# Optimization experiments

Hardware: AMD Instinct MI355X
Metric: run time of the kernel (lower is better)

## Reference

```python
import jax, jax.numpy as jnp
import numpy as np

N_QUBITS = 10
DEPTH = 2
CNOT_PATTERN = [(i, i + 1) for i in range(N_QUBITS - 1)] + [(N_QUBITS - 1, 0)]

def _signs(n):
    # Pauli-Z eigenvalue (+1/-1) of each basis state for each wire; wire 0 = MSB
    idx = np.arange(2 ** n)
    bits = (idx[:, None] >> np.arange(n - 1, -1, -1)[None, :]) & 1
    return jnp.asarray(1.0 - 2.0 * bits, jnp.float32)  # [2^n, n]

SIGNS = _signs(N_QUBITS)

def _apply_rx(s, theta, wire):
    # s: [B, 2,2,...,2] complex; RX(theta) = [[c, -i s],[-i s, c]], c=cos(theta/2)
    s0 = jnp.take(s, 0, axis=wire + 1)
    s1 = jnp.take(s, 1, axis=wire + 1)
    c = jnp.cos(theta * 0.5)
    sn = jnp.sin(theta * 0.5)
    if c.ndim:  # per-batch angle -> broadcast over remaining wire axes
        shp = (-1,) + (1,) * (s0.ndim - 1)
        c = c.reshape(shp)
        sn = sn.reshape(shp)
    return jnp.stack([c * s0 - 1j * sn * s1, -1j * sn * s0 + c * s1], axis=wire + 1)

def _apply_cnot(s, src, tgt):
    # flip target wire on the src=1 subspace (X gate == flip of the size-2 axis)
    s0 = jnp.take(s, 0, axis=src + 1)
    s1 = jnp.take(s, 1, axis=src + 1)
    t_ax = tgt + 1 - (1 if tgt > src else 0)  # target axis after removing src axis
    s1 = jnp.flip(s1, axis=t_ax)
    return jnp.stack([s0, s1], axis=src + 1)

def _qgate(x, rx_params):
    # x: [B, n_qubits] data angles -> PauliZ expectations [B, n_qubits]
    B = x.shape[0]
    n = N_QUBITS
    s = jnp.zeros((B, 2 ** n), jnp.complex64).at[:, 0].set(1.0)
    s = s.reshape((B,) + (2,) * n)
    for w in range(n):
        s = _apply_rx(s, x[:, w], w)
    for _ in range(DEPTH):
        for w in range(n):
            s = _apply_rx(s, rx_params[w], w)
        for src, tgt in CNOT_PATTERN:
            s = _apply_cnot(s, src, tgt)
    probs = jnp.abs(s.reshape(B, -1)) ** 2  # [B, 2^n]
    return probs @ SIGNS  # [B, n]


def setup_inputs():
    key = jax.random.key(0)
    ks = jax.random.split(key, 10)
    T, B, D, H = 256, 256, 128, N_QUBITS
    fan_in = D + H
    sc = 1.0 / np.sqrt(fan_in)
    def lin(k1, k2):
        W = jax.random.uniform(k1, (H, fan_in), jnp.float32, -sc, sc)
        b = jax.random.uniform(k2, (H,), jnp.float32, -sc, sc)
        return W, b
    inputs = jax.random.normal(ks[0], (T, B, D), jnp.float32)
    rx_params = jax.random.normal(ks[1], (H,), jnp.float32)
    Wf, bf = lin(ks[2], ks[3])
    Wi, bi = lin(ks[4], ks[5])
    Wg, bg = lin(ks[6], ks[7])
    Wo, bo = lin(ks[8], ks[9])
    return dict(inputs=inputs, rx_params=rx_params, Wf=Wf, bf=bf, Wi=Wi, bi=bi,
                Wg=Wg, bg=bg, Wo=Wo, bo=bo)


def reference(inputs, rx_params, Wf, bf, Wi, bi, Wg, bg, Wo, bo):
    T, B, _ = inputs.shape
    H = N_QUBITS
    def step(carry, x_t):
        hx, cx = carry
        comb = jnp.concatenate([x_t, hx], axis=1)  # [B, D+H]
        f = jax.nn.sigmoid(_qgate(comb @ Wf.T + bf, rx_params))
        i = jax.nn.sigmoid(_qgate(comb @ Wi.T + bi, rx_params))
        g = jnp.tanh(_qgate(comb @ Wg.T + bg, rx_params))
        o = jax.nn.sigmoid(_qgate(comb @ Wo.T + bo, rx_params))
        cx = f * cx + i * g
        hx = o * jnp.tanh(cx)
        return (hx, cx), hx
    h0 = jnp.zeros((B, H), inputs.dtype)
    c0 = jnp.zeros((B, H), inputs.dtype)
    (hT, cT), ys = jax.lax.scan(step, (h0, c0), inputs)
    return ys, hT, cT
```

## Files before the change

kernel.cpp:

```cpp
#include <hip/hip_runtime.h>
#include <math.h>

#define T_STEPS 256
#define BATCH   256
#define DDIM    128
#define NH      10

typedef float v2f __attribute__((ext_vector_type(2)));
__device__ __forceinline__ v2f sp(float x){ v2f r; r.x = x; r.y = x; return r; }
#define PKFMA(a,b,c) __builtin_elementwise_fma((a),(b),(c))

template<int CTRL, int RMASK, int BMASK>
__device__ __forceinline__ float dppz(float x){
  return __int_as_float(__builtin_amdgcn_update_dpp(
      0, __float_as_int(x), CTRL, RMASK, BMASK, true));
}
__device__ __forceinline__ float red63(float v){
  v += dppz<0x111, 0xF, 0xF>(v);
  v += dppz<0x112, 0xF, 0xF>(v);
  v += dppz<0x114, 0xF, 0xE>(v);
  v += dppz<0x118, 0xF, 0xC>(v);
  v += dppz<0x142, 0xA, 0xF>(v);
  v += dppz<0x143, 0xC, 0xF>(v);
  return v;
}
__device__ __forceinline__ float rdlane(float v, int l){
  return __int_as_float(__builtin_amdgcn_readlane(__float_as_int(v), l));
}

template<int CTRL,int RMASK,int BMASK>
__device__ __forceinline__ float lad_add(float v){ return v + dppz<CTRL,RMASK,BMASK>(v); }
template<int CTRL,int RMASK,int BMASK>
__device__ __forceinline__ float lad_sub(float v){ return dppz<CTRL,RMASK,BMASK>(v) - v; }
#define LAD0_A(v) lad_add<0x111,0xF,0xF>(v)
#define LAD0_S(v) lad_sub<0x111,0xF,0xF>(v)
#define LAD1_A(v) lad_add<0x112,0xF,0xF>(v)
#define LAD1_S(v) lad_sub<0x112,0xF,0xF>(v)
#define LAD2_A(v) lad_add<0x114,0xF,0xE>(v)
#define LAD2_S(v) lad_sub<0x114,0xF,0xE>(v)
#define LAD3_A(v) lad_add<0x118,0xF,0xC>(v)
#define LAD3_S(v) lad_sub<0x118,0xF,0xC>(v)
#define LAD4_A(v) lad_add<0x142,0xA,0xF>(v)
#define LAD4_S(v) lad_sub<0x142,0xA,0xF>(v)
#define LAD5_A(v) lad_add<0x143,0xC,0xF>(v)
#define LAD5_S(v) lad_sub<0x143,0xC,0xF>(v)

__device__ __forceinline__ float dsx32(float x){ return __shfl_xor(x, 32, 64); }
__device__ __forceinline__ float dsx16(float x){
  return __int_as_float(__builtin_amdgcn_ds_swizzle(__float_as_int(x), 0x401F));
}
__device__ __forceinline__ float dsx8(float x){
  return __int_as_float(__builtin_amdgcn_ds_swizzle(__float_as_int(x), 0x201F));
}
__device__ __forceinline__ float dsx4(float x){
  return __int_as_float(__builtin_amdgcn_ds_swizzle(__float_as_int(x), 0x101F));
}
__device__ __forceinline__ float dsx2(float x){
  return __int_as_float(__builtin_amdgcn_ds_swizzle(__float_as_int(x), 0x081F));
}
__device__ __forceinline__ float dsx1(float x){
  return __int_as_float(__builtin_amdgcn_ds_swizzle(__float_as_int(x), 0x041F));
}

#define NK 4

#define RX_LANE_T(FETCH, tv)                                                   \
  { const v2f tt_ = sp(tv), nt_ = sp(-(tv));                                   \
    _Pragma("unroll")                                                          \
    for (int k = 0; k < NK; ++k){                                              \
      v2f oa, ob;                                                              \
      oa.x = FETCH(RE[k].x); oa.y = FETCH(RE[k].y);                            \
      ob.x = FETCH(IM[k].x); ob.y = FETCH(IM[k].y);                            \
      RE[k] = PKFMA(tt_, ob, RE[k]);                                           \
      IM[k] = PKFMA(nt_, oa, IM[k]);                                           \
    } }

template<int XB>
__device__ __forceinline__ void rx_reg_t(float tv, v2f* RE, v2f* IM){
  const v2f tt = sp(tv), nt = sp(-tv);
  v2f oR[NK], oI[NK];
  #pragma unroll
  for (int k = 0; k < NK; ++k){ oR[k] = RE[k]; oI[k] = IM[k]; }
  #pragma unroll
  for (int k = 0; k < NK; ++k){
    RE[k] = PKFMA(tt, oI[k ^ XB], RE[k]);
    IM[k] = PKFMA(nt, oR[k ^ XB], IM[k]);
  }
}
__device__ __forceinline__ void rx_reg9_t(float tv, v2f* RE, v2f* IM){
  const v2f tt = sp(tv), nt = sp(-tv);
  #pragma unroll
  for (int k = 0; k < NK; ++k){
    v2f oa = __builtin_shufflevector(RE[k], RE[k], 1, 0);
    v2f ob = __builtin_shufflevector(IM[k], IM[k], 1, 0);
    RE[k] = PKFMA(tt, ob, RE[k]);
    IM[k] = PKFMA(nt, oa, IM[k]);
  }
}

__device__ __forceinline__ void xdots(float xa, float xb,
                                      const v2f* WA, const v2f* WB, float* s){
  v2f xav = sp(xa), xbv = sp(xb);
  v2f p0 = PKFMA(xav, WA[0], xbv * WB[0]);
  v2f p1 = PKFMA(xav, WA[1], xbv * WB[1]);
  v2f p2 = PKFMA(xav, WA[2], xbv * WB[2]);
  s[0] = red63(p0.x); s[1] = red63(p0.y);
  s[2] = red63(p1.x); s[3] = red63(p1.y);
  s[4] = red63(p2.x);
}

__global__ void __launch_bounds__(512)
__attribute__((amdgpu_waves_per_eu(2)))
qlstm_kernel(const float* __restrict__ inp, const float* __restrict__ rxp,
             const float* __restrict__ Wf, const float* __restrict__ bf,
             const float* __restrict__ Wi, const float* __restrict__ bi,
             const float* __restrict__ Wg, const float* __restrict__ bg,
             const float* __restrict__ Wo, const float* __restrict__ bo,
             float* __restrict__ out)
{
  const int b    = blockIdx.x;
  const int tid  = threadIdx.x;
  const int wv   = tid >> 6;
  const int g    = wv >> 1;
  const int half = wv & 1;
  const int lane = tid & 63;

  __shared__ float4 Sx[4][2][4][64];
  __shared__ float4 partv[2][64];
  __shared__ float xpub_s[4][16];
  ((float*)partv)[tid] = 0.f;

  const float* Wp = (g == 0) ? Wf : (g == 1) ? Wi : (g == 2) ? Wg : Wo;
  const float* bp = (g == 0) ? bf : (g == 1) ? bi : (g == 2) ? bg : bo;

  const float WSC = 0.07957747154594767f;

  const int wbase = half * 5;
  v2f WA[3], WB[3];
  float bq[5];
  #pragma unroll
  for (int k = 0; k < 5; ++k) bq[k] = WSC * (bp[wbase + k] + rxp[wbase + k]);
  #pragma unroll
  for (int j = 0; j < 3; ++j){
    const int w0 = wbase + 2*j, w1 = wbase + 2*j + 1;
    WA[j].x = WSC * Wp[w0*138 + lane];
    WB[j].x = WSC * Wp[w0*138 + 64 + lane];
    if (2*j + 1 < 5){
      WA[j].y = WSC * Wp[w1*138 + lane];
      WB[j].y = WSC * Wp[w1*138 + 64 + lane];
    } else { WA[j].y = 0.f; WB[j].y = 0.f; }
  }
  float wCT[NH];
  {
    const int row = (lane < NH) ? lane : 0;
    #pragma unroll
    for (int j = 0; j < NH; ++j){
      float v = WSC * Wp[row*138 + 128 + j];
      wCT[j] = (lane < NH) ? v : 0.f;
    }
  }

  float tq[NH];
  float PC = 1.f;
  #pragma unroll
  for (int w = 0; w < NH; ++w){
    float th = 0.5f * rxp[w];
    float cw = cosf(th), sw = sinf(th);
    PC *= cw;
    tq[w] = sw / cw;
  }

  const int l5 = (lane>>5)&1, l4 = (lane>>4)&1, l3 = (lane>>3)&1;
  const int l2 = (lane>>2)&1, l1 = (lane>>1)&1, l0 = lane&1;
  const int pb2 = l4^l3, pb3 = l3^l2, pb4 = l2^l1, pb5 = l1^l0;
  const int a0 = l5, a1 = l5^l4;
  const int a6w = l0 ^ half;
  const int n_base = pb2 + pb3 + pb4 + pb5 + a6w;

  v2f CRE[NK], CIM[NK];
  #pragma unroll
  for (int r = 0; r < 2*NK; ++r){
    const int R0 = r&1, R1 = (r>>1)&1, R2 = (r>>2)&1;
    int k = (n_base + (a0^R0) + (a1^R0) + (half^R2) + (R2^R1) + (R1^R0)) & 3;
    float cr = (k==0) ? PC : (k==2) ? -PC : 0.f;
    float ci = (k==1) ? -PC : (k==3) ? PC : 0.f;
    if (R0){ CRE[r>>1].y = cr; CIM[r>>1].y = ci; }
    else   { CRE[r>>1].x = cr; CIM[r>>1].x = ci; }
  }

  const float sig = (lane == 0 || lane >= 6) ? -1.f : 1.f;

  float h = 0.f, c = 0.f;

  const float* x0 = inp + (size_t)b * DDIM;
  float xa = x0[lane];
  float xb = x0[64 + lane];

  {
    float sx[5];
    xdots(xa, xb, WA, WB, sx);
    if (lane == 63){
      #pragma unroll
      for (int k = 0; k < 5; ++k) xpub_s[g][wbase + k] = sx[k] + bq[k];
    }
  }
  __syncthreads();

  #pragma unroll 1
  for (int t = 0; t < T_STEPS; ++t){
    if (t + 1 < T_STEPS){
      const float* nx = inp + ((size_t)(t+1) * BATCH + b) * DDIM;
      xa = nx[lane];
      xb = nx[64 + lane];
    }

    float cs[NH], sn[NH];
    {
      float xr = xpub_s[g][lane & 15];
      float hdA = rdlane(h, 0) * wCT[0];
      float hdB = rdlane(h, 1) * wCT[1];
      hdA = fmaf(rdlane(h, 2), wCT[2], hdA);
      hdB = fmaf(rdlane(h, 3), wCT[3], hdB);
      hdA = fmaf(rdlane(h, 4), wCT[4], hdA);
      hdB = fmaf(rdlane(h, 5), wCT[5], hdB);
      hdA = fmaf(rdlane(h, 6), wCT[6], hdA);
      hdB = fmaf(rdlane(h, 7), wCT[7], hdB);
      hdA = fmaf(rdlane(h, 8), wCT[8], hdA);
      hdB = fmaf(rdlane(h, 9), wCT[9], hdB);
      float th = xr + (hdA + hdB);
      float cA = __builtin_amdgcn_cosf(th);
      float sA = __builtin_amdgcn_sinf(th);
      #pragma unroll
      for (int w = 0; w < NH; ++w){
        cs[w] = rdlane(cA, w);
        sn[w] = rdlane(sA, w);
      }
    }

    float f2 = pb2 ? sn[2] : cs[2];
    float f3 = pb3 ? sn[3] : cs[3];
    float f4 = pb4 ? sn[4] : cs[4];
    float f5 = pb5 ? sn[5] : cs[5];
    float m2345 = ((f2*f3)*(f4*f5)) * (a6w ? sn[6] : cs[6]);

    float q0 = (a0 ? sn[0] : cs[0]) * (a1 ? sn[1] : cs[1]);
    float q1 = (a0 ? cs[0] : sn[0]) * (a1 ? cs[1] : sn[1]);
    v2f ZZ; ZZ.x = m2345 * q0; ZZ.y = m2345 * q1;

    float u7  = half ? sn[7] : cs[7];
    float u7b = half ? cs[7] : sn[7];
    float t78[4];
    t78[0] = u7  * cs[8];
    t78[1] = u7  * sn[8];
    t78[2] = u7b * sn[8];
    t78[3] = u7b * cs[8];

    v2f s9a; s9a.x = cs[9]; s9a.y = sn[9];
    v2f s9b; s9b.x = sn[9]; s9b.y = cs[9];

    v2f RE[NK], IM[NK];
    #pragma unroll
    for (int k = 0; k < NK; ++k){
      v2f M = (sp(t78[k]) * ((k & 1) ? s9b : s9a)) * ZZ;
      RE[k] = M * CRE[k];
      IM[k] = M * CIM[k];
    }

    RX_LANE_T(dsx32, tq[0])
    RX_LANE_T(dsx16, tq[1])
    RX_LANE_T(dsx8,  tq[2])
    RX_LANE_T(dsx4,  tq[3])
    RX_LANE_T(dsx2,  tq[4])
    RX_LANE_T(dsx1,  tq[5])
    rx_reg_t<2>(tq[7], RE, IM);
    rx_reg_t<1>(tq[8], RE, IM);
    rx_reg9_t  (tq[9], RE, IM);

    Sx[g][half][0][lane] = make_float4(RE[0].x, RE[0].y, RE[1].x, RE[1].y);
    Sx[g][half][1][lane] = make_float4(RE[2].x, RE[2].y, RE[3].x, RE[3].y);
    Sx[g][half][2][lane] = make_float4(IM[0].x, IM[0].y, IM[1].x, IM[1].y);
    Sx[g][half][3][lane] = make_float4(IM[2].x, IM[2].y, IM[3].x, IM[3].y);

    float sx[5];
    xdots(xa, xb, WA, WB, sx);

    __syncthreads();
    {
      float4 pr0 = Sx[g][half^1][0][lane];
      float4 pr1 = Sx[g][half^1][1][lane];
      float4 pi0 = Sx[g][half^1][2][lane];
      float4 pi1 = Sx[g][half^1][3][lane];
      v2f PR[NK], PI[NK];
      PR[0].x = pr0.x; PR[0].y = pr0.y; PR[1].x = pr0.z; PR[1].y = pr0.w;
      PR[2].x = pr1.x; PR[2].y = pr1.y; PR[3].x = pr1.z; PR[3].y = pr1.w;
      PI[0].x = pi0.x; PI[0].y = pi0.y; PI[1].x = pi0.z; PI[1].y = pi0.w;
      PI[2].x = pi1.x; PI[2].y = pi1.y; PI[3].x = pi1.z; PI[3].y = pi1.w;
      const v2f t6 = sp(tq[6]), n6 = sp(-tq[6]);
      #pragma unroll
      for (int k = 0; k < NK; ++k){
        RE[k] = PKFMA(t6, PI[k], RE[k]);
        IM[k] = PKFMA(n6, PR[k], IM[k]);
      }
    }

    v2f Pk[NK];
    #pragma unroll
    for (int k = 0; k < NK; ++k) Pk[k] = PKFMA(RE[k], RE[k], IM[k] * IM[k]);
    float A0 = Pk[0].x + Pk[0].y, A1 = Pk[1].x + Pk[1].y;
    float A2 = Pk[2].x + Pk[2].y, A3 = Pk[3].x + Pk[3].y;
    float B0 = Pk[0].x - Pk[0].y, B1 = Pk[1].x - Pk[1].y;
    float B2 = Pk[2].x - Pk[2].y, B3 = Pk[3].x - Pk[3].y;
    float su = A0 + A1, sv = A2 + A3;
    float tot = su + sv;
    float q4  = su - sv;
    float q6  = (A0 - A1) - (A2 - A3);
    float q7  = (B0 - B1) - (B2 - B3);

    float a0p = LAD0_A(tot);
    float a0m = LAD0_S(tot);
    float b1pp = LAD1_A(a0p);
    float b1pm = LAD1_S(a0p);
    float b1mm = LAD1_S(a0m);
    float c2ppp = LAD2_A(b1pp);
    float c2ppm = LAD2_S(b1pp);
    float c2pmm = LAD2_S(b1pm);
    float c2mmm = LAD2_S(b1mm);
    float d1 = LAD3_A(c2ppp);
    float d2 = LAD3_S(c2ppp);
    float d3 = LAD3_S(c2ppm);
    float d4 = LAD3_S(c2pmm);
    float d5 = LAD3_S(c2mmm);
    float P1 = LAD5_S(LAD4_S(d1));
    float P2 = LAD5_S(LAD4_S(d2));
    float P3 = LAD5_S(LAD4_S(d3));
    float P4 = LAD5_S(LAD4_S(d4));
    float P5 = LAD5_S(LAD4_S(d5));
    float e = LAD0_S(q7);
    e = LAD1_S(e); e = LAD2_S(e); e = LAD3_S(e); e = LAD4_S(e);
    float P9 = LAD5_S(e);
    float P0 = LAD5_A(e);
    float f_ = LAD0_S(q4);
    f_ = LAD1_S(f_); f_ = LAD2_S(f_); f_ = LAD3_S(f_); f_ = LAD4_S(f_);
    float P7 = LAD5_S(f_);
    float g_ = LAD0_S(q6);
    g_ = LAD1_S(g_); g_ = LAD2_S(g_); g_ = LAD3_S(g_); g_ = LAD4_S(g_);
    float P8 = LAD5_S(g_);

    if (lane == 63){
      float vals[10] = {P0,P1,P2,P3,P4,P5,P5,P7,P8,P9};
      #pragma unroll
      for (int j = 0; j < 10; ++j)
        ((float*)&partv[half][j])[g] = vals[j];
      #pragma unroll
      for (int k = 0; k < 5; ++k)
        xpub_s[g][wbase + k] = sx[k] + bq[k];
    }
    __syncthreads();

    float4 eL = partv[0][lane];
    float4 eH = partv[1][lane];
    float E0 = fmaf(sig, eH.x, eL.x);
    float E1 = fmaf(sig, eH.y, eL.y);
    float E2 = fmaf(sig, eH.z, eL.z);
    float E3 = fmaf(sig, eH.w, eL.w);
    float fv = 1.f / (1.f + __expf(-E0));
    float iv = 1.f / (1.f + __expf(-E1));
    float e2g = __expf(2.f * E2);
    float gv = (e2g - 1.f) / (e2g + 1.f);
    float ov = 1.f / (1.f + __expf(-E3));
    c = fmaf(fv, c, iv * gv);
    float e2c = __expf(2.f * c);
    h = ov * ((e2c - 1.f) / (e2c + 1.f));

    if (wv == 0 && lane < NH)
      out[((size_t)t * BATCH + b) * NH + lane] = h;
  }

  if (wv == 0 && lane < NH){
    const size_t ysN = (size_t)T_STEPS * BATCH * NH;
    out[ysN + (size_t)b * NH + lane]                      = h;
    out[ysN + (size_t)BATCH * NH + (size_t)b * NH + lane] = c;
  }
}

extern "C" void kernel_launch(void* const* d_in, const int* in_sizes, int n_in,
                              void* d_out, int out_size, void* d_ws, size_t ws_size,
                              hipStream_t stream)
{
  qlstm_kernel<<<BATCH, 512, 0, stream>>>(
      (const float*)d_in[0], (const float*)d_in[1],
      (const float*)d_in[2], (const float*)d_in[3],
      (const float*)d_in[4], (const float*)d_in[5],
      (const float*)d_in[6], (const float*)d_in[7],
      (const float*)d_in[8], (const float*)d_in[9],
      (float*)d_out);
}
```

Measured before the change: 788.8 us.

## Compute wire-6 RX partner contribution locally instead of exchanging via LDS

The RX gate on wire 6 was applied by writing each half-wave's amplitudes to shared memory, synchronizing the block, and reading the partner half's values. Because the initial state is a product state, the partner half's amplitudes can be formed locally from the complementary cos/sin factor for wire 6 plus precomputed phase and sign coefficients. This removes a __syncthreads and the 16 KB LDS exchange from each timestep, in exchange for extra packed FMAs and registers per step. Correctness depends on the wire-6 RX commuting with the later per-lane and per-register RX gates that now run before it.

```diff
diff --git a/kernel.cpp b/kernel.cpp
--- a/kernel.cpp
+++ b/kernel.cpp
@@ -125,7 +125,6 @@
   const int half = wv & 1;
   const int lane = tid & 63;
 
-  __shared__ float4 Sx[4][2][4][64];
   __shared__ float4 partv[2][64];
   __shared__ float xpub_s[4][16];
   ((float*)partv)[tid] = 0.f;
@@ -177,15 +176,20 @@
   const int a6w = l0 ^ half;
   const int n_base = pb2 + pb3 + pb4 + pb5 + a6w;
 
-  v2f CRE[NK], CIM[NK];
+  v2f CRE[NK], CIM[NK], D6RE[NK], D6IM[NK];
   #pragma unroll
   for (int r = 0; r < 2*NK; ++r){
     const int R0 = r&1, R1 = (r>>1)&1, R2 = (r>>2)&1;
     int k = (n_base + (a0^R0) + (a1^R0) + (half^R2) + (R2^R1) + (R1^R0)) & 3;
     float cr = (k==0) ? PC : (k==2) ? -PC : 0.f;
     float ci = (k==1) ? -PC : (k==3) ? PC : 0.f;
-    if (R0){ CRE[r>>1].y = cr; CIM[r>>1].y = ci; }
-    else   { CRE[r>>1].x = cr; CIM[r>>1].x = ci; }
+    float sg6 = ((l0 ^ R2) & 1) ? tq[6] : -tq[6];
+    float dre = sg6 * ci;
+    float dim = -sg6 * cr;
+    if (R0){ CRE[r>>1].y = cr;  CIM[r>>1].y = ci;
+             D6RE[r>>1].y = dre; D6IM[r>>1].y = dim; }
+    else   { CRE[r>>1].x = cr;  CIM[r>>1].x = ci;
+             D6RE[r>>1].x = dre; D6IM[r>>1].x = dim; }
   }
 
   const float sig = (lane == 0 || lane >= 6) ? -1.f : 1.f;
@@ -241,11 +245,16 @@
     float f3 = pb3 ? sn[3] : cs[3];
     float f4 = pb4 ? sn[4] : cs[4];
     float f5 = pb5 ? sn[5] : cs[5];
-    float m2345 = ((f2*f3)*(f4*f5)) * (a6w ? sn[6] : cs[6]);
+    float m2345b = (f2*f3)*(f4*f5);
+    float w6o = a6w ? sn[6] : cs[6];
+    float w6p = a6w ? cs[6] : sn[6];
+    float mo = m2345b * w6o;
+    float mp = m2345b * w6p;
 
     float q0 = (a0 ? sn[0] : cs[0]) * (a1 ? sn[1] : cs[1]);
     float q1 = (a0 ? cs[0] : sn[0]) * (a1 ? cs[1] : sn[1]);
-    v2f ZZ; ZZ.x = m2345 * q0; ZZ.y = m2345 * q1;
+    v2f ZZ; ZZ.x = mo * q0; ZZ.y = mo * q1;
+    v2f ZP; ZP.x = mp * q0; ZP.y = mp * q1;
 
     float u7  = half ? sn[7] : cs[7];
     float u7b = half ? cs[7] : sn[7];
@@ -261,9 +270,11 @@
     v2f RE[NK], IM[NK];
     #pragma unroll
     for (int k = 0; k < NK; ++k){
-      v2f M = (sp(t78[k]) * ((k & 1) ? s9b : s9a)) * ZZ;
-      RE[k] = M * CRE[k];
-      IM[k] = M * CIM[k];
+      v2f s9v = (k & 1) ? s9b : s9a;
+      v2f M  = (sp(t78[k])     * s9v) * ZZ;
+      v2f Mp = (sp(t78[k ^ 3]) * s9v) * ZP;
+      RE[k] = PKFMA(Mp, D6RE[k], M * CRE[k]);
+      IM[k] = PKFMA(Mp, D6IM[k], M * CIM[k]);
     }
 
     RX_LANE_T(dsx32, tq[0])
@@ -276,32 +287,8 @@
     rx_reg_t<1>(tq[8], RE, IM);
     rx_reg9_t  (tq[9], RE, IM);
 
-    Sx[g][half][0][lane] = make_float4(RE[0].x, RE[0].y, RE[1].x, RE[1].y);
-    Sx[g][half][1][lane] = make_float4(RE[2].x, RE[2].y, RE[3].x, RE[3].y);
-    Sx[g][half][2][lane] = make_float4(IM[0].x, IM[0].y, IM[1].x, IM[1].y);
-    Sx[g][half][3][lane] = make_float4(IM[2].x, IM[2].y, IM[3].x, IM[3].y);
-
     float sx[5];
     xdots(xa, xb, WA, WB, sx);
-
-    __syncthreads();
-    {
-      float4 pr0 = Sx[g][half^1][0][lane];
-      float4 pr1 = Sx[g][half^1][1][lane];
-      float4 pi0 = Sx[g][half^1][2][lane];
-      float4 pi1 = Sx[g][half^1][3][lane];
-      v2f PR[NK], PI[NK];
-      PR[0].x = pr0.x; PR[0].y = pr0.y; PR[1].x = pr0.z; PR[1].y = pr0.w;
-      PR[2].x = pr1.x; PR[2].y = pr1.y; PR[3].x = pr1.z; PR[3].y = pr1.w;
-      PI[0].x = pi0.x; PI[0].y = pi0.y; PI[1].x = pi0.z; PI[1].y = pi0.w;
-      PI[2].x = pi1.x; PI[2].y = pi1.y; PI[3].x = pi1.z; PI[3].y = pi1.w;
-      const v2f t6 = sp(tq[6]), n6 = sp(-tq[6]);
-      #pragma unroll
-      for (int k = 0; k < NK; ++k){
-        RE[k] = PKFMA(t6, PI[k], RE[k]);
-        IM[k] = PKFMA(n6, PR[k], IM[k]);
-      }
-    }
 
     v2f Pk[NK];
     #pragma unroll
```

Result: faster. 753.5 us (-4.5%).
